# Kernel tuning notes

Hardware: AMD Instinct MI355X
Metric: run time of the kernel (lower is better)

The kernel has to match this reference:

```python
import jax, jax.numpy as jnp
import numpy as np

WH, WW = 7, 7
SH, SW = 3, 3
NUM_HEADS = 8


def _rel_pos_index(wh, ww):
    coords = np.stack(np.meshgrid(np.arange(wh), np.arange(ww), indexing='ij')).reshape(2, -1)
    rel = (coords[:, :, None] - coords[:, None, :]).transpose(1, 2, 0)  # [N,N,2]
    rel[..., 0] += wh - 1
    rel[..., 1] += ww - 1
    rel[..., 0] *= 2 * ww - 1
    return rel.sum(-1)  # [N,N] int


def _attn_mask(Hp, Wp, wh, ww, sh, sw):
    img = np.zeros((Hp, Wp), dtype=np.float32)
    cnt = 0
    for hs in (slice(0, -wh), slice(-wh, -sh), slice(-sh, None)):
        for ws in (slice(0, -ww), slice(-ww, -sw), slice(-sw, None)):
            img[hs, ws] = cnt
            cnt += 1
    win = img.reshape(Hp // wh, wh, Wp // ww, ww).transpose(0, 2, 1, 3).reshape(-1, wh * ww)  # [nW,N]
    diff = win[:, None, :] - win[:, :, None]  # [nW,N,N]
    return np.where(diff != 0, -100.0, 0.0).astype(np.float32)


def _layernorm(x, g, b, eps=1e-5):
    mu = jnp.mean(x, -1, keepdims=True)
    var = jnp.mean(jnp.square(x - mu), -1, keepdims=True)
    return (x - mu) * jax.lax.rsqrt(var + eps) * g + b


def setup_inputs() -> dict:
    key = jax.random.key(0)
    ks = jax.random.split(key, 12)
    B, H, W, C = 32, 56, 56, 256
    hid = 4 * C
    s = lambda k, *shape: jax.random.normal(k, shape, jnp.float32) * 0.02
    return {
        'x': jax.random.normal(ks[0], (B, H * W, C), jnp.float32),
        'g1': jnp.ones((C,), jnp.float32), 'b1': jnp.zeros((C,), jnp.float32),
        'qkv_w': s(ks[1], 3 * C, C), 'qkv_b': jnp.zeros((3 * C,), jnp.float32),
        'bias_table': s(ks[2], (2 * WH - 1) * (2 * WW - 1), NUM_HEADS),
        'proj_w': s(ks[3], C, C), 'proj_b': jnp.zeros((C,), jnp.float32),
        'g2': jnp.ones((C,), jnp.float32), 'b2': jnp.zeros((C,), jnp.float32),
        'w1': s(ks[4], hid, C), 'bm1': jnp.zeros((hid,), jnp.float32),
        'w2': s(ks[5], C, hid), 'bm2': jnp.zeros((C,), jnp.float32),
        'H': H, 'W': W,
    }


def reference(x, g1, b1, qkv_w, qkv_b, bias_table, proj_w, proj_b, g2, b2, w1, bm1, w2, bm2, H, W):
    B, L, C = x.shape
    wh, ww = WH, WW
    nH = NUM_HEADS
    hd = C // nH
    scale = hd ** -0.5
    N = wh * ww

    shortcut = x
    h = _layernorm(x, g1, b1).reshape(B, H, W, C)
    pad_b = (wh - H % wh) % wh
    pad_r = (ww - W % ww) % ww
    if pad_b or pad_r:
        h = jnp.pad(h, ((0, 0), (0, pad_b), (0, pad_r), (0, 0)))
    Hp, Wp = h.shape[1], h.shape[2]

    h = jnp.roll(h, (-SH, -SW), axis=(1, 2))
    # window partition -> [B*nW, N, C]
    nWh, nWw = Hp // wh, Wp // ww
    xw = h.reshape(B, nWh, wh, nWw, ww, C).transpose(0, 1, 3, 2, 4, 5).reshape(-1, N, C)

    qkv = jnp.einsum('bnc,oc->bno', xw, qkv_w) + qkv_b  # [B*nW, N, 3C]
    qkv = qkv.reshape(-1, N, 3, nH, hd).transpose(2, 0, 3, 1, 4)
    q, k, v = qkv[0] * scale, qkv[1], qkv[2]  # [B*nW, nH, N, hd]
    attn = jnp.einsum('whnd,whmd->whnm', q, k)  # [B*nW, nH, N, N]

    rpi = jnp.asarray(_rel_pos_index(wh, ww))
    bias = bias_table[rpi.reshape(-1)].reshape(N, N, nH).transpose(2, 0, 1)  # [nH,N,N]
    attn = attn + bias[None]

    mask = jnp.asarray(_attn_mask(Hp, Wp, wh, ww, SH, SW))  # [nW,N,N]
    nW = mask.shape[0]
    attn = attn.reshape(B, nW, nH, N, N) + mask[None, :, None]
    attn = jax.nn.softmax(attn.reshape(-1, nH, N, N), axis=-1)

    out = jnp.einsum('whnm,whmd->whnd', attn, v).transpose(0, 2, 1, 3).reshape(-1, N, C)
    out = jnp.einsum('bnc,oc->bno', out, proj_w) + proj_b

    # window reverse
    out = out.reshape(B, nWh, nWw, wh, ww, C).transpose(0, 1, 3, 2, 4, 5).reshape(B, Hp, Wp, C)
    out = jnp.roll(out, (SH, SW), axis=(1, 2))
    if pad_b or pad_r:
        out = out[:, :H, :W, :]
    out = out.reshape(B, H * W, C)

    x = shortcut + out
    m = _layernorm(x, g2, b2)
    m = jax.nn.gelu(jnp.einsum('blc,oc->blo', m, w1) + bm1, approximate=False)
    m = jnp.einsum('blh,oh->blo', m, w2) + bm2
    return x + m
```

## Files before the change

kernel.cpp:

```cpp
#include <hip/hip_runtime.h>
#include <hip/hip_bf16.h>

#define DEVI __device__ __forceinline__
#define AS1 __attribute__((address_space(1)))
#define AS3 __attribute__((address_space(3)))

typedef short bf16x8 __attribute__((ext_vector_type(8)));
typedef float f32x4  __attribute__((ext_vector_type(4)));
typedef unsigned short u16x4 __attribute__((ext_vector_type(4)));

constexpr int MROWS = 100352;

DEVI int win_row_to_token(int r) {
  int b   = r / 3136;
  int rem = r - b * 3136;
  int wi  = rem / 49;
  int t   = rem - wi * 49;
  int nwh = wi >> 3, nww = wi & 7;
  int th = t / 7, tw = t - th * 7;
  int h = nwh * 7 + th + 3; if (h >= 56) h -= 56;
  int w = nww * 7 + tw + 3; if (w >= 56) w -= 56;
  return b * 3136 + h * 56 + w;
}

DEVI unsigned short f2bf(float f) {
  __hip_bfloat16 h = __float2bfloat16(f);
  return __builtin_bit_cast(unsigned short, h);
}

DEVI float gelu_t(float v) {
  float u2 = v * (1.5957691216f + 0.1426930877f * v * v);
  float e  = __expf(u2);
  return v * e / (e + 1.0f);
}

__global__ void pack_kernel(const float* __restrict__ W, __hip_bfloat16* __restrict__ Wp,
                            int N, int K) {
  long t = (long)blockIdx.x * 256 + threadIdx.x;
  long total = (long)N * K / 8;
  if (t >= total) return;
  int l  = (int)(t & 63);
  long f = t >> 6;
  int ni = (int)(f & 3);
  int kk = (int)((f >> 2) & 7);
  long r = f >> 5;
  int KB = K / 256;
  int kb = (int)(r % KB);
  int nb = (int)(r / KB);
  int row  = nb * 64 + (l & 15) + ni * 16;
  int col0 = kb * 256 + kk * 32 + (l >> 4) * 8;
  const float* src = W + (size_t)row * K + col0;
  u16x4 lo, hi;
  #pragma unroll
  for (int e = 0; e < 4; ++e) { lo[e] = f2bf(src[e]); hi[e] = f2bf(src[4 + e]); }
  *(u16x4*)(Wp + t * 8)     = lo;
  *(u16x4*)(Wp + t * 8 + 4) = hi;
}

__global__ __launch_bounds__(256) void ln_kernel(
    const float* __restrict__ xin, const float* __restrict__ g,
    const float* __restrict__ b, __hip_bfloat16* __restrict__ outb)
{
  int r = blockIdx.x * 4 + (threadIdx.x >> 6);
  int l = threadIdx.x & 63;
  int tok = win_row_to_token(r);
  float4 xv = *(const float4*)&xin[(size_t)tok * 256 + l * 4];
  float s = xv.x + xv.y + xv.z + xv.w;
  float q = xv.x * xv.x + xv.y * xv.y + xv.z * xv.z + xv.w * xv.w;
  #pragma unroll
  for (int off = 32; off; off >>= 1) { s += __shfl_xor(s, off); q += __shfl_xor(q, off); }
  float mu = s * (1.0f / 256.0f);
  float var = q * (1.0f / 256.0f) - mu * mu;
  float rs = rsqrtf(var + 1e-5f);
  float4 gv = *(const float4*)&g[l * 4];
  float4 bv = *(const float4*)&b[l * 4];
  ushort4 st;
  st.x = f2bf((xv.x - mu) * rs * gv.x + bv.x);
  st.y = f2bf((xv.y - mu) * rs * gv.y + bv.y);
  st.z = f2bf((xv.z - mu) * rs * gv.z + bv.z);
  st.w = f2bf((xv.w - mu) * rs * gv.w + bv.w);
  *(ushort4*)&outb[(size_t)r * 256 + l * 4] = st;
}

__global__ __launch_bounds__(256, 3) void gemm_qkv(
    const __hip_bfloat16* __restrict__ A,
    const __hip_bfloat16* __restrict__ Wp,
    const float* __restrict__ bias,
    __hip_bfloat16* __restrict__ outb)
{
  constexpr int CB = 3;
  __shared__ __align__(16) __hip_bfloat16 Al[64 * 256];

  const int tid = threadIdx.x;
  const int w = tid >> 6, l = tid & 63;
  const int g = l >> 4, lm = l & 15;

  const int nwg = gridDim.x;
  int bswz = (blockIdx.x & 7) * (nwg >> 3) + (blockIdx.x >> 3);
  const int mt = bswz / CB;
  const int cb = bswz - mt * CB;

  const char* At = (const char*)A + (size_t)mt * 64 * 512;
  char* AlB = (char*)Al;
  const int r0  = tid >> 5;
  const int usw = ((tid & 31) ^ r0) << 4;
  const int lmx = lm & 7;
  const int arow = lm * 512;

  const __hip_bfloat16* WpB = Wp + (size_t)(cb * 4 + w) * 16384;
  const int colb = cb * 256 + w * 64 + g * 4;

  f32x4 acc[4][4];
  {
    f32x4 bias_v[4];
    #pragma unroll
    for (int ni = 0; ni < 4; ++ni) bias_v[ni] = *(const f32x4*)&bias[colb + ni * 16];
    #pragma unroll
    for (int mi = 0; mi < 4; ++mi)
      #pragma unroll
      for (int ni = 0; ni < 4; ++ni) acc[mi][ni] = bias_v[ni];
  }

  #pragma unroll
  for (int j = 0; j < 8; ++j)
    __builtin_amdgcn_global_load_lds(
        (const AS1 void*)(At + (long)(j * 8 + r0) * 512 + usw),
        (AS3 void*)(AlB + j * 4096 + w * 1024), 16, 0, 0);
  asm volatile("s_waitcnt vmcnt(0)" ::: "memory");
  __syncthreads();

  #pragma unroll
  for (int kk = 0; kk < 8; ++kk) {
    bf16x8 bf[4], af[4];
    #pragma unroll
    for (int ni = 0; ni < 4; ++ni)
      bf[ni] = *(const bf16x8*)(WpB + ((kk * 4 + ni) * 64 + l) * 8);
    #pragma unroll
    for (int mi = 0; mi < 4; ++mi)
      af[mi] = *(const bf16x8*)(AlB + arow + mi * 8192 + ((((kk << 2) | g) ^ lmx) << 4));
    #pragma unroll
    for (int mi = 0; mi < 4; ++mi)
      #pragma unroll
      for (int ni = 0; ni < 4; ++ni)
        acc[mi][ni] = __builtin_amdgcn_mfma_f32_16x16x32_bf16(bf[ni], af[mi], acc[mi][ni], 0, 0, 0);
  }

  #pragma unroll
  for (int mi = 0; mi < 4; ++mi) {
    int grow = mt * 64 + mi * 16 + lm;
    __hip_bfloat16* rp = outb + (size_t)grow * 768 + colb;
    #pragma unroll
    for (int ni = 0; ni < 4; ++ni) {
      u16x4 st = { f2bf(acc[mi][ni][0]), f2bf(acc[mi][ni][1]),
                   f2bf(acc[mi][ni][2]), f2bf(acc[mi][ni][3]) };
      *(u16x4*)(rp + ni * 16) = st;
    }
  }
}

__global__ __launch_bounds__(256, 3) void proj_ln2(
    const __hip_bfloat16* __restrict__ A,
    const __hip_bfloat16* __restrict__ Wp,
    const float* __restrict__ bias,
    const float* __restrict__ xres,
    const float* __restrict__ g2, const float* __restrict__ b2,
    float* __restrict__ outf,
    __hip_bfloat16* __restrict__ alnout)
{
  __shared__ __align__(16) __hip_bfloat16 Al[64 * 256];
  __shared__ float2 Sst[4][16][4];

  const int tid = threadIdx.x;
  const int w = tid >> 6, l = tid & 63;
  const int g = l >> 4, lm = l & 15;

  const int nwg = gridDim.x;
  int bswz = (blockIdx.x & 7) * (nwg >> 3) + (blockIdx.x >> 3);
  const int mt = bswz;

  const char* At = (const char*)A + (size_t)mt * 64 * 512;
  char* AlB = (char*)Al;
  const int r0  = tid >> 5;
  const int usw = ((tid & 31) ^ r0) << 4;
  const int lmx = lm & 7;
  const int arow = lm * 512;

  const __hip_bfloat16* WpB = Wp + (size_t)w * 16384;
  const int colb = w * 64 + g * 4;

  f32x4 acc[4][4];
  {
    f32x4 bias_v[4];
    #pragma unroll
    for (int ni = 0; ni < 4; ++ni) bias_v[ni] = *(const f32x4*)&bias[colb + ni * 16];
    #pragma unroll
    for (int mi = 0; mi < 4; ++mi)
      #pragma unroll
      for (int ni = 0; ni < 4; ++ni) acc[mi][ni] = bias_v[ni];
  }

  #pragma unroll
  for (int j = 0; j < 8; ++j)
    __builtin_amdgcn_global_load_lds(
        (const AS1 void*)(At + (long)(j * 8 + r0) * 512 + usw),
        (AS3 void*)(AlB + j * 4096 + w * 1024), 16, 0, 0);
  asm volatile("s_waitcnt vmcnt(0)" ::: "memory");
  __syncthreads();

  #pragma unroll
  for (int kk = 0; kk < 8; ++kk) {
    bf16x8 bf[4], af[4];
    #pragma unroll
    for (int ni = 0; ni < 4; ++ni)
      bf[ni] = *(const bf16x8*)(WpB + ((kk * 4 + ni) * 64 + l) * 8);
    #pragma unroll
    for (int mi = 0; mi < 4; ++mi)
      af[mi] = *(const bf16x8*)(AlB + arow + mi * 8192 + ((((kk << 2) | g) ^ lmx) << 4));
    #pragma unroll
    for (int mi = 0; mi < 4; ++mi)
      #pragma unroll
      for (int ni = 0; ni < 4; ++ni)
        acc[mi][ni] = __builtin_amdgcn_mfma_f32_16x16x32_bf16(bf[ni], af[mi], acc[mi][ni], 0, 0, 0);
  }

  int orow_[4];
  #pragma unroll
  for (int mi = 0; mi < 4; ++mi) {
    int grow = mt * 64 + mi * 16 + lm;
    int orow = win_row_to_token(grow);
    orow_[mi] = orow;
    const f32x4* xr = (const f32x4*)(xres + (size_t)orow * 256 + colb);
    f32x4* op = (f32x4*)(outf + (size_t)orow * 256 + colb);
    float s = 0.0f, sq = 0.0f;
    #pragma unroll
    for (int ni = 0; ni < 4; ++ni) {
      f32x4 r = xr[ni * 4] + acc[mi][ni];
      acc[mi][ni] = r;
      op[ni * 4] = r;
      #pragma unroll
      for (int j = 0; j < 4; ++j) { s += r[j]; sq += r[j] * r[j]; }
    }
    s  += __shfl_xor(s, 16);  sq += __shfl_xor(sq, 16);
    s  += __shfl_xor(s, 32);  sq += __shfl_xor(sq, 32);
    if (g == 0) Sst[mi][lm][w] = float2{s, sq};
  }
  __syncthreads();

  f32x4 g2v[4], b2v[4];
  #pragma unroll
  for (int ni = 0; ni < 4; ++ni) {
    g2v[ni] = *(const f32x4*)&g2[colb + ni * 16];
    b2v[ni] = *(const f32x4*)&b2[colb + ni * 16];
  }
  #pragma unroll
  for (int mi = 0; mi < 4; ++mi) {
    float s = 0.0f, sq = 0.0f;
    #pragma unroll
    for (int ww = 0; ww < 4; ++ww) { float2 t = Sst[mi][lm][ww]; s += t.x; sq += t.y; }
    float mu = s * (1.0f / 256.0f);
    float rs = rsqrtf(sq * (1.0f / 256.0f) - mu * mu + 1e-5f);
    __hip_bfloat16* ap = alnout + (size_t)orow_[mi] * 256 + colb;
    #pragma unroll
    for (int ni = 0; ni < 4; ++ni) {
      u16x4 st;
      #pragma unroll
      for (int j = 0; j < 4; ++j)
        st[j] = f2bf((acc[mi][ni][j] - mu) * rs * g2v[ni][j] + b2v[ni][j]);
      *(u16x4*)(ap + ni * 16) = st;
    }
  }
}

__global__ __launch_bounds__(512, 2) void mlp_fused(
    const __hip_bfloat16* __restrict__ A,
    const __hip_bfloat16* __restrict__ W1p,
    const __hip_bfloat16* __restrict__ W2p,
    const float* __restrict__ bm1, const float* __restrict__ bm2,
    float* __restrict__ outf)
{
  __shared__ __align__(16) __hip_bfloat16 Al[64 * 256];
  __shared__ __align__(16) __hip_bfloat16 Hl[64 * 256];

  const int tid = threadIdx.x;
  const int w = tid >> 6, l = tid & 63;
  const int g = l >> 4, lm = l & 15;
  const int wr = w >> 2, wc = w & 3;

  const int nwg = gridDim.x;
  int bswz = (blockIdx.x & 7) * (nwg >> 3) + (blockIdx.x >> 3);
  const int mt = bswz;

  const char* At = (const char*)A + (size_t)mt * 64 * 512;
  char* AlB = (char*)Al;
  char* HlB = (char*)Hl;
  const int usw = ((tid & 31) ^ ((tid >> 5) & 7)) << 4;
  const int lmx = lm & 7;
  const int arow = (wr * 32 + lm) * 512;
  const int colb = wc * 64 + g * 4;

  #pragma unroll
  for (int j = 0; j < 4; ++j)
    __builtin_amdgcn_global_load_lds(
        (const AS1 void*)(At + (long)(j * 16 + (tid >> 5)) * 512 + usw),
        (AS3 void*)(AlB + j * 8192 + w * 1024), 16, 0, 0);
  asm volatile("s_waitcnt vmcnt(0)" ::: "memory");
  __syncthreads();

  f32x4 acc2[2][4];
  {
    f32x4 b2v[4];
    #pragma unroll
    for (int ni = 0; ni < 4; ++ni) b2v[ni] = *(const f32x4*)&bm2[colb + ni * 16];
    #pragma unroll
    for (int mi = 0; mi < 2; ++mi)
      #pragma unroll
      for (int ni = 0; ni < 4; ++ni) acc2[mi][ni] = b2v[ni];
  }

  #pragma unroll
  for (int q = 0; q < 4; ++q) {
    f32x4 acc1[2][4];
    {
      f32x4 b1v[4];
      #pragma unroll
      for (int ni = 0; ni < 4; ++ni) b1v[ni] = *(const f32x4*)&bm1[q * 256 + colb + ni * 16];
      #pragma unroll
      for (int mi = 0; mi < 2; ++mi)
        #pragma unroll
        for (int ni = 0; ni < 4; ++ni) acc1[mi][ni] = b1v[ni];
    }
    const __hip_bfloat16* Wk1 = W1p + (size_t)(q * 4 + wc) * 16384;
    #pragma unroll
    for (int kk = 0; kk < 8; ++kk) {
      bf16x8 bf[4], af[2];
      #pragma unroll
      for (int ni = 0; ni < 4; ++ni)
        bf[ni] = *(const bf16x8*)(Wk1 + ((kk * 4 + ni) * 64 + l) * 8);
      #pragma unroll
      for (int mi = 0; mi < 2; ++mi)
        af[mi] = *(const bf16x8*)(AlB + arow + mi * 8192 + ((((kk << 2) | g) ^ lmx) << 4));
      #pragma unroll
      for (int mi = 0; mi < 2; ++mi)
        #pragma unroll
        for (int ni = 0; ni < 4; ++ni)
          acc1[mi][ni] = __builtin_amdgcn_mfma_f32_16x16x32_bf16(bf[ni], af[mi], acc1[mi][ni], 0, 0, 0);
    }

    __syncthreads();
    #pragma unroll
    for (int mi = 0; mi < 2; ++mi) {
      int rowb = arow + mi * 8192;
      #pragma unroll
      for (int ni = 0; ni < 4; ++ni) {
        u16x4 hv = { f2bf(gelu_t(acc1[mi][ni][0])), f2bf(gelu_t(acc1[mi][ni][1])),
                     f2bf(gelu_t(acc1[mi][ni][2])), f2bf(gelu_t(acc1[mi][ni][3])) };
        int unit = (wc * 8 + ni * 2 + (g >> 1)) ^ lmx;
        *(u16x4*)(HlB + rowb + unit * 16 + (g & 1) * 8) = hv;
      }
    }
    __syncthreads();

    const __hip_bfloat16* Wk2 = W2p + (size_t)(wc * 4 + q) * 16384;
    #pragma unroll
    for (int kk = 0; kk < 8; ++kk) {
      bf16x8 bf[4], af[2];
      #pragma unroll
      for (int ni = 0; ni < 4; ++ni)
        bf[ni] = *(const bf16x8*)(Wk2 + ((kk * 4 + ni) * 64 + l) * 8);
      #pragma unroll
      for (int mi = 0; mi < 2; ++mi)
        af[mi] = *(const bf16x8*)(HlB + arow + mi * 8192 + ((((kk << 2) | g) ^ lmx) << 4));
      #pragma unroll
      for (int mi = 0; mi < 2; ++mi)
        #pragma unroll
        for (int ni = 0; ni < 4; ++ni)
          acc2[mi][ni] = __builtin_amdgcn_mfma_f32_16x16x32_bf16(bf[ni], af[mi], acc2[mi][ni], 0, 0, 0);
    }
  }

  #pragma unroll
  for (int mi = 0; mi < 2; ++mi) {
    int grow = mt * 64 + wr * 32 + mi * 16 + lm;
    f32x4* op = (f32x4*)(outf + (size_t)grow * 256 + colb);
    #pragma unroll
    for (int ni = 0; ni < 4; ++ni)
      op[ni * 4] = op[ni * 4] + acc2[mi][ni];
  }
}

__global__ __launch_bounds__(256) void bias_prep_kernel(
    const float* __restrict__ bt, float* __restrict__ Sadd)
{
  int blk = blockIdx.x;
  int cls = blk >> 3, h = blk & 7;
  int re = cls >> 1, ce = cls & 1;
  int lane = threadIdx.x & 63, fs = threadIdx.x >> 6;
  int g = lane >> 4, lm = lane & 15;
  #pragma unroll
  for (int i = 0; i < 4; ++i) {
    int f = fs * 4 + i;
    int mi = f >> 2, ni = f & 3;
    int key = ni * 16 + lm;
    f32x4 v;
    #pragma unroll
    for (int j = 0; j < 4; ++j) {
      int q = mi * 16 + g * 4 + j;
      float val;
      if (key >= 49) {
        val = -1e30f;
      } else {
        int qq = q > 48 ? 48 : q;
        int qh = qq / 7, qw = qq - qh * 7;
        int kh = key / 7, kw = key - kh * 7;
        int rpi = (qh - kh + 6) * 13 + (qw - kw + 6);
        val = bt[rpi * 8 + h];
        int rq = (re ? (qh < 4 ? 1 : 2) : 0) * 3 + (ce ? (qw < 4 ? 1 : 2) : 0);
        int rk = (re ? (kh < 4 ? 1 : 2) : 0) * 3 + (ce ? (kw < 4 ? 1 : 2) : 0);
        if (rq != rk) val -= 100.0f;
      }
      v[j] = val;
    }
    ((f32x4*)Sadd)[(blk * 16 + f) * 64 + lane] = v;
  }
}

__global__ __launch_bounds__(256) void attn_mfma_kernel(
    const __hip_bfloat16* __restrict__ qkv,
    const float* __restrict__ Sadd,
    __hip_bfloat16* __restrict__ attn_out)
{
  __shared__ __align__(16) __hip_bfloat16 Pl[4][64 * 72];
  int blk = blockIdx.x;
  int win = blk >> 1, half = blk & 1;
  int w = threadIdx.x >> 6, l = threadIdx.x & 63;
  int head = half * 4 + w;
  int g = l >> 4, lm = l & 15;
  int wi = win & 63;
  int cls = (((wi >> 3) == 7) ? 2 : 0) | (((wi & 7) == 7) ? 1 : 0);
  const __hip_bfloat16* base = qkv + (size_t)win * 49 * 768 + head * 32;

  bf16x8 aQ[4], bK[4];
  #pragma unroll
  for (int mi = 0; mi < 4; ++mi) {
    int q = mi * 16 + lm; if (q > 48) q = 48;
    aQ[mi] = *(const bf16x8*)(base + q * 768 + g * 8);
  }
  #pragma unroll
  for (int ni = 0; ni < 4; ++ni) {
    int k = ni * 16 + lm; if (k > 48) k = 48;
    bK[ni] = *(const bf16x8*)(base + 256 + k * 768 + g * 8);
  }
  f32x4 acc[4][4] = {};
  #pragma unroll
  for (int mi = 0; mi < 4; ++mi)
    #pragma unroll
    for (int ni = 0; ni < 4; ++ni)
      acc[mi][ni] = __builtin_amdgcn_mfma_f32_16x16x32_bf16(aQ[mi], bK[ni], acc[mi][ni], 0, 0, 0);

  const float scale = 0.17677669529663687f;
  const f32x4* Sb = (const f32x4*)Sadd + (size_t)(cls * 8 + head) * 16 * 64 + l;

  f32x4 rsum[4];
  __hip_bfloat16* P = Pl[w];
  #pragma unroll
  for (int mi = 0; mi < 4; ++mi) {
    #pragma unroll
    for (int ni = 0; ni < 4; ++ni) {
      f32x4 sv = Sb[(mi * 4 + ni) * 64];
      #pragma unroll
      for (int j = 0; j < 4; ++j) acc[mi][ni][j] = acc[mi][ni][j] * scale + sv[j];
    }
    f32x4 mx = acc[mi][0];
    #pragma unroll
    for (int ni = 1; ni < 4; ++ni)
      #pragma unroll
      for (int j = 0; j < 4; ++j) mx[j] = fmaxf(mx[j], acc[mi][ni][j]);
    #pragma unroll
    for (int msk = 1; msk < 16; msk <<= 1)
      #pragma unroll
      for (int j = 0; j < 4; ++j) mx[j] = fmaxf(mx[j], __shfl_xor(mx[j], msk));
    f32x4 sm = {};
    #pragma unroll
    for (int ni = 0; ni < 4; ++ni)
      #pragma unroll
      for (int j = 0; j < 4; ++j) {
        float e = __expf(acc[mi][ni][j] - mx[j]);
        acc[mi][ni][j] = e;
        sm[j] += e;
      }
    #pragma unroll
    for (int msk = 1; msk < 16; msk <<= 1)
      #pragma unroll
      for (int j = 0; j < 4; ++j) sm[j] += __shfl_xor(sm[j], msk);
    rsum[mi] = sm;
    #pragma unroll
    for (int ni = 0; ni < 4; ++ni)
      #pragma unroll
      for (int j = 0; j < 4; ++j) {
        int q = mi * 16 + g * 4 + j;
        int key = ni * 16 + lm;
        P[q * 72 + key] = __float2bfloat16(acc[mi][ni][j]);
      }
  }

  bf16x8 bV[2][2];
  #pragma unroll
  for (int s = 0; s < 2; ++s)
    #pragma unroll
    for (int n2 = 0; n2 < 2; ++n2) {
      bf16x8 vv;
      #pragma unroll
      for (int e = 0; e < 8; ++e) {
        int key = s * 32 + g * 8 + e; if (key > 48) key = 48;
        vv[e] = __builtin_bit_cast(short, base[512 + key * 768 + n2 * 16 + lm]);
      }
      bV[s][n2] = vv;
    }

  f32x4 o[4][2] = {};
  #pragma unroll
  for (int s = 0; s < 2; ++s)
    #pragma unroll
    for (int mi2 = 0; mi2 < 4; ++mi2) {
      bf16x8 aP = *(const bf16x8*)&P[(mi2 * 16 + lm) * 72 + s * 32 + g * 8];
      #pragma unroll
      for (int n2 = 0; n2 < 2; ++n2)
        o[mi2][n2] = __builtin_amdgcn_mfma_f32_16x16x32_bf16(aP, bV[s][n2], o[mi2][n2], 0, 0, 0);
    }

  #pragma unroll
  for (int mi2 = 0; mi2 < 4; ++mi2) {
    f32x4 li;
    #pragma unroll
    for (int j = 0; j < 4; ++j) li[j] = 1.0f / rsum[mi2][j];
    #pragma unroll
    for (int n2 = 0; n2 < 2; ++n2)
      #pragma unroll
      for (int j = 0; j < 4; ++j) {
        int q = mi2 * 16 + g * 4 + j;
        if (q < 49)
          attn_out[((size_t)win * 49 + q) * 256 + head * 32 + n2 * 16 + lm] =
              __float2bfloat16(o[mi2][n2][j] * li[j]);
      }
  }
}

extern "C" void kernel_launch(void* const* d_in, const int* in_sizes, int n_in,
                              void* d_out, int out_size, void* d_ws, size_t ws_size,
                              hipStream_t stream) {
  const float* x          = (const float*)d_in[0];
  const float* g1         = (const float*)d_in[1];
  const float* b1         = (const float*)d_in[2];
  const float* qkv_w      = (const float*)d_in[3];
  const float* qkv_b      = (const float*)d_in[4];
  const float* bias_table = (const float*)d_in[5];
  const float* proj_w     = (const float*)d_in[6];
  const float* proj_b     = (const float*)d_in[7];
  const float* g2         = (const float*)d_in[8];
  const float* b2         = (const float*)d_in[9];
  const float* w1         = (const float*)d_in[10];
  const float* bm1        = (const float*)d_in[11];
  const float* w2         = (const float*)d_in[12];
  const float* bm2        = (const float*)d_in[13];
  float* out = (float*)d_out;

  char* ws = (char*)d_ws;
  __hip_bfloat16* A_ln   = (__hip_bfloat16*)(ws);
  __hip_bfloat16* qkvb   = (__hip_bfloat16*)(ws + 51380224);
  __hip_bfloat16* attn_o = (__hip_bfloat16*)(ws + 205520896);
  __hip_bfloat16* qkv_wb  = (__hip_bfloat16*)(ws + 256901120);
  __hip_bfloat16* proj_wb = qkv_wb + 196608;
  __hip_bfloat16* w1b     = proj_wb + 65536;
  __hip_bfloat16* w2b     = w1b + 262144;
  float* Sadd = (float*)(ws + 258473984);

  pack_kernel<<<(196608 / 8 + 255) / 256, 256, 0, stream>>>(qkv_w, qkv_wb, 768, 256);
  pack_kernel<<<(65536  / 8 + 255) / 256, 256, 0, stream>>>(proj_w, proj_wb, 256, 256);
  pack_kernel<<<(262144 / 8 + 255) / 256, 256, 0, stream>>>(w1, w1b, 1024, 256);
  pack_kernel<<<(262144 / 8 + 255) / 256, 256, 0, stream>>>(w2, w2b, 256, 1024);
  bias_prep_kernel<<<32, 256, 0, stream>>>(bias_table, Sadd);

  ln_kernel<<<MROWS / 4, 256, 0, stream>>>(x, g1, b1, A_ln);

  gemm_qkv<<<1568 * 3, 256, 0, stream>>>(A_ln, qkv_wb, qkv_b, qkvb);

  attn_mfma_kernel<<<4096, 256, 0, stream>>>(qkvb, Sadd, attn_o);

  proj_ln2<<<1568, 256, 0, stream>>>(attn_o, proj_wb, proj_b, x, g2, b2, out, A_ln);

  mlp_fused<<<1568, 512, 0, stream>>>(A_ln, w1b, w2b, bm1, bm2, out);
}
```

Measured before the change: 487.2 us.

## Enlarge fused MLP row tile to 128 and halve weight fragment loads per wave

```diff
diff --git a/kernel.cpp b/kernel.cpp
--- a/kernel.cpp
+++ b/kernel.cpp
@@ -271,120 +271,122 @@
   }
 }
 
-__global__ __launch_bounds__(512, 2) void mlp_fused(
+__global__ __launch_bounds__(512, 1) void mlp_fused(
     const __hip_bfloat16* __restrict__ A,
     const __hip_bfloat16* __restrict__ W1p,
     const __hip_bfloat16* __restrict__ W2p,
     const float* __restrict__ bm1, const float* __restrict__ bm2,
     float* __restrict__ outf)
 {
-  __shared__ __align__(16) __hip_bfloat16 Al[64 * 256];
-  __shared__ __align__(16) __hip_bfloat16 Hl[64 * 256];
+  __shared__ __align__(16) __hip_bfloat16 Al[128 * 256];
+  __shared__ __align__(16) __hip_bfloat16 Hl[128 * 256];
 
   const int tid = threadIdx.x;
   const int w = tid >> 6, l = tid & 63;
   const int g = l >> 4, lm = l & 15;
-  const int wr = w >> 2, wc = w & 3;
 
   const int nwg = gridDim.x;
   int bswz = (blockIdx.x & 7) * (nwg >> 3) + (blockIdx.x >> 3);
   const int mt = bswz;
 
-  const char* At = (const char*)A + (size_t)mt * 64 * 512;
+  const char* At = (const char*)A + (size_t)mt * 128 * 512;
   char* AlB = (char*)Al;
   char* HlB = (char*)Hl;
-  const int usw = ((tid & 31) ^ ((tid >> 5) & 7)) << 4;
   const int lmx = lm & 7;
-  const int arow = (wr * 32 + lm) * 512;
-  const int colb = wc * 64 + g * 4;
-
-  #pragma unroll
-  for (int j = 0; j < 4; ++j)
-    __builtin_amdgcn_global_load_lds(
-        (const AS1 void*)(At + (long)(j * 16 + (tid >> 5)) * 512 + usw),
-        (AS3 void*)(AlB + j * 8192 + w * 1024), 16, 0, 0);
+  const int arow = lm * 512;
+  const int nbase = (w & 1) * 2;
+  const int colb = w * 32 + g * 4;
+
+  {
+    const int r0 = tid >> 5;
+    const int usw = ((tid & 31) ^ (r0 & 7)) << 4;
+    #pragma unroll
+    for (int j = 0; j < 8; ++j)
+      __builtin_amdgcn_global_load_lds(
+          (const AS1 void*)(At + (long)(j * 16 + r0) * 512 + usw),
+          (AS3 void*)(AlB + j * 8192 + w * 1024), 16, 0, 0);
+  }
   asm volatile("s_waitcnt vmcnt(0)" ::: "memory");
   __syncthreads();
 
-  f32x4 acc2[2][4];
+  f32x4 acc2[8][2];
   {
-    f32x4 b2v[4];
-    #pragma unroll
-    for (int ni = 0; ni < 4; ++ni) b2v[ni] = *(const f32x4*)&bm2[colb + ni * 16];
-    #pragma unroll
-    for (int mi = 0; mi < 2; ++mi)
-      #pragma unroll
-      for (int ni = 0; ni < 4; ++ni) acc2[mi][ni] = b2v[ni];
+    f32x4 b2v[2];
+    #pragma unroll
+    for (int ni2 = 0; ni2 < 2; ++ni2) b2v[ni2] = *(const f32x4*)&bm2[colb + ni2 * 16];
+    #pragma unroll
+    for (int mi = 0; mi < 8; ++mi)
+      #pragma unroll
+      for (int ni2 = 0; ni2 < 2; ++ni2) acc2[mi][ni2] = b2v[ni2];
   }
 
   #pragma unroll
   for (int q = 0; q < 4; ++q) {
-    f32x4 acc1[2][4];
+    f32x4 acc1[8][2];
     {
-      f32x4 b1v[4];
-      #pragma unroll
-      for (int ni = 0; ni < 4; ++ni) b1v[ni] = *(const f32x4*)&bm1[q * 256 + colb + ni * 16];
-      #pragma unroll
-      for (int mi = 0; mi < 2; ++mi)
+      f32x4 b1v[2];
+      #pragma unroll
+      for (int ni2 = 0; ni2 < 2; ++ni2)
+        b1v[ni2] = *(const f32x4*)&bm1[q * 256 + colb + ni2 * 16];
+      #pragma unroll
+      for (int mi = 0; mi < 8; ++mi)
         #pragma unroll
-        for (int ni = 0; ni < 4; ++ni) acc1[mi][ni] = b1v[ni];
-    }
-    const __hip_bfloat16* Wk1 = W1p + (size_t)(q * 4 + wc) * 16384;
+        for (int ni2 = 0; ni2 < 2; ++ni2) acc1[mi][ni2] = b1v[ni2];
+    }
+    const __hip_bfloat16* Wk1 = W1p + (size_t)(q * 4 + (w >> 1)) * 16384;
     #pragma unroll
     for (int kk = 0; kk < 8; ++kk) {
-      bf16x8 bf[4], af[2];
-      #pragma unroll
-      for (int ni = 0; ni < 4; ++ni)
-        bf[ni] = *(const bf16x8*)(Wk1 + ((kk * 4 + ni) * 64 + l) * 8);
-      #pragma unroll
-      for (int mi = 0; mi < 2; ++mi)
-        af[mi] = *(const bf16x8*)(AlB + arow + mi * 8192 + ((((kk << 2) | g) ^ lmx) << 4));
-      #pragma unroll
-      for (int mi = 0; mi < 2; ++mi)
+      bf16x8 bf[2];
+      #pragma unroll
+      for (int ni2 = 0; ni2 < 2; ++ni2)
+        bf[ni2] = *(const bf16x8*)(Wk1 + ((kk * 4 + nbase + ni2) * 64 + l) * 8);
+      #pragma unroll
+      for (int mi = 0; mi < 8; ++mi) {
+        bf16x8 af = *(const bf16x8*)(AlB + arow + mi * 8192 + ((((kk << 2) | g) ^ lmx) << 4));
         #pragma unroll
-        for (int ni = 0; ni < 4; ++ni)
-          acc1[mi][ni] = __builtin_amdgcn_mfma_f32_16x16x32_bf16(bf[ni], af[mi], acc1[mi][ni], 0, 0, 0);
+        for (int ni2 = 0; ni2 < 2; ++ni2)
+          acc1[mi][ni2] = __builtin_amdgcn_mfma_f32_16x16x32_bf16(bf[ni2], af, acc1[mi][ni2], 0, 0, 0);
+      }
     }
 
     __syncthreads();
     #pragma unroll
-    for (int mi = 0; mi < 2; ++mi) {
+    for (int mi = 0; mi < 8; ++mi) {
       int rowb = arow + mi * 8192;
       #pragma unroll
-      for (int ni = 0; ni < 4; ++ni) {
-        u16x4 hv = { f2bf(gelu_t(acc1[mi][ni][0])), f2bf(gelu_t(acc1[mi][ni][1])),
-                     f2bf(gelu_t(acc1[mi][ni][2])), f2bf(gelu_t(acc1[mi][ni][3])) };
-        int unit = (wc * 8 + ni * 2 + (g >> 1)) ^ lmx;
+      for (int ni2 = 0; ni2 < 2; ++ni2) {
+        u16x4 hv = { f2bf(gelu_t(acc1[mi][ni2][0])), f2bf(gelu_t(acc1[mi][ni2][1])),
+                     f2bf(gelu_t(acc1[mi][ni2][2])), f2bf(gelu_t(acc1[mi][ni2][3])) };
+        int unit = (w * 4 + ni2 * 2 + (g >> 1)) ^ lmx;
         *(u16x4*)(HlB + rowb + unit * 16 + (g & 1) * 8) = hv;
       }
     }
     __syncthreads();
 
-    const __hip_bfloat16* Wk2 = W2p + (size_t)(wc * 4 + q) * 16384;
+    const __hip_bfloat16* Wk2 = W2p + (size_t)((w >> 1) * 4 + q) * 16384;
     #pragma unroll
     for (int kk = 0; kk < 8; ++kk) {
-      bf16x8 bf[4], af[2];
-      #pragma unroll
-      for (int ni = 0; ni < 4; ++ni)
-        bf[ni] = *(const bf16x8*)(Wk2 + ((kk * 4 + ni) * 64 + l) * 8);
-      #pragma unroll
-      for (int mi = 0; mi < 2; ++mi)
-        af[mi] = *(const bf16x8*)(HlB + arow + mi * 8192 + ((((kk << 2) | g) ^ lmx) << 4));
-      #pragma unroll
-      for (int mi = 0; mi < 2; ++mi)
+      bf16x8 bf[2];
+      #pragma unroll
+      for (int ni2 = 0; ni2 < 2; ++ni2)
+        bf[ni2] = *(const bf16x8*)(Wk2 + ((kk * 4 + nbase + ni2) * 64 + l) * 8);
+      #pragma unroll
+      for (int mi = 0; mi < 8; ++mi) {
+        bf16x8 af = *(const bf16x8*)(HlB + arow + mi * 8192 + ((((kk << 2) | g) ^ lmx) << 4));
         #pragma unroll
-        for (int ni = 0; ni < 4; ++ni)
-          acc2[mi][ni] = __builtin_amdgcn_mfma_f32_16x16x32_bf16(bf[ni], af[mi], acc2[mi][ni], 0, 0, 0);
-    }
-  }
-
-  #pragma unroll
-  for (int mi = 0; mi < 2; ++mi) {
-    int grow = mt * 64 + wr * 32 + mi * 16 + lm;
+        for (int ni2 = 0; ni2 < 2; ++ni2)
+          acc2[mi][ni2] = __builtin_amdgcn_mfma_f32_16x16x32_bf16(bf[ni2], af, acc2[mi][ni2], 0, 0, 0);
+      }
+    }
+  }
+
+  #pragma unroll
+  for (int mi = 0; mi < 8; ++mi) {
+    int grow = mt * 128 + mi * 16 + lm;
     f32x4* op = (f32x4*)(outf + (size_t)grow * 256 + colb);
     #pragma unroll
-    for (int ni = 0; ni < 4; ++ni)
-      op[ni * 4] = op[ni * 4] + acc2[mi][ni];
+    for (int ni2 = 0; ni2 < 2; ++ni2)
+      op[ni2 * 4] = op[ni2 * 4] + acc2[mi][ni2];
   }
 }
 
@@ -588,5 +590,5 @@
 
   proj_ln2<<<1568, 256, 0, stream>>>(attn_o, proj_wb, proj_b, x, g2, b2, out, A_ln);
 
-  mlp_fused<<<1568, 512, 0, stream>>>(A_ln, w1b, w2b, bm1, bm2, out);
-}
+  mlp_fused<<<784, 512, 0, stream>>>(A_ln, w1b, w2b, bm1, bm2, out);
+}
```

New measurement: 474.2 us. 2.7% less time.
